# Kernel tuning notes

Measured on AMD Instinct MI355X. Metric: run time of the kernel, lower is better.

Reference implementation:

```python
import jax, jax.numpy as jnp
import numpy as np

K = 10
ALPHA = 0.1
N_NODES = 100000
N_EDGES = 3200000
IN_CH, HID_CH, OUT_CH = 500, 64, 16


def setup_inputs() -> dict:
    key = jax.random.key(0)
    k1, k2, k3, k4, k5, k6 = jax.random.split(key, 6)
    x = jax.random.normal(k1, (N_NODES, IN_CH), dtype=jnp.float32)
    edge_index = jax.random.randint(k2, (2, N_EDGES), 0, N_NODES, dtype=jnp.int64)
    # Linear params (Kaiming-uniform-ish scale)
    s1 = 1.0 / np.sqrt(IN_CH)
    s2 = 1.0 / np.sqrt(HID_CH)
    W1 = jax.random.uniform(k3, (IN_CH, HID_CH), dtype=jnp.float32, minval=-s1, maxval=s1)
    b1 = jax.random.uniform(k4, (HID_CH,), dtype=jnp.float32, minval=-s1, maxval=s1)
    W2 = jax.random.uniform(k5, (HID_CH, OUT_CH), dtype=jnp.float32, minval=-s2, maxval=s2)
    b2 = jax.random.uniform(k6, (OUT_CH,), dtype=jnp.float32, minval=-s2, maxval=s2)
    return {"x": x, "edge_index": edge_index, "W1": W1, "b1": b1, "W2": W2, "b2": b2}


def reference(x, edge_index, W1, b1, W2, b2):
    N = x.shape[0]
    # MLP (eval mode: dropout is identity)
    h = jnp.maximum(x @ W1 + b1, 0.0)
    h = h @ W2 + b2  # [N, out_channels]

    # GCN normalization with self-loops (PyG gcn_norm defaults)
    loops = jnp.arange(N, dtype=edge_index.dtype)
    row = jnp.concatenate([edge_index[0], loops])  # source
    col = jnp.concatenate([edge_index[1], loops])  # target
    ones = jnp.ones(row.shape[0], dtype=h.dtype)
    deg = jax.ops.segment_sum(ones, col, num_segments=N)
    dinv = jnp.where(deg > 0, jax.lax.rsqrt(deg), 0.0)
    norm = dinv[row] * dinv[col]  # [E+N]

    # K-step APPNP propagation: h_{k+1} = (1-alpha) * A_hat h_k + alpha * h_0
    h0 = h

    def step(_, hk):
        agg = jax.ops.segment_sum(norm[:, None] * hk[row], col, num_segments=N)
        return (1.0 - ALPHA) * agg + ALPHA * h0

    return jax.lax.fori_loop(0, K, step, h)
```

## Files before the change

### kernel.cpp

```cpp
#include <hip/hip_runtime.h>

#define IN_CH 500
#define KSTEPS 10

typedef unsigned int u32;
typedef unsigned short u16;
typedef short bf16x8 __attribute__((ext_vector_type(8)));
typedef float f32x4 __attribute__((ext_vector_type(4)));

__device__ __forceinline__ float bf2f(u16 u) {
    union { u32 i; float f; } v; v.i = ((u32)u) << 16; return v.f;
}
__device__ __forceinline__ u16 f2bf(float f) {
    union { float f; u32 i; } v; v.f = f;
    u32 x = v.i;
    return (u16)((x + 0x7FFFu + ((x >> 16) & 1u)) >> 16);
}
__device__ __forceinline__ u32 f_as_u(float f) {
    union { float f; u32 i; } v; v.f = f; return v.i;
}
__device__ __forceinline__ float u_as_f(u32 i) {
    union { u32 i; float f; } v; v.i = i; return v.f;
}

__global__ void detect_kernel(const u16* __restrict__ w1raw,
                              const int* __restrict__ ei,
                              u32* __restrict__ flags) {
    int t = threadIdx.x;
    float m = fabsf(bf2f(w1raw[t]));
    m = fmaxf(m, fabsf(bf2f(w1raw[64 + t])));
    m = fmaxf(m, fabsf(bf2f(w1raw[128 + t])));
    for (int off = 32; off; off >>= 1) m = fmaxf(m, __shfl_down(m, off));
    u32 o = (u32)ei[2 * t + 1];
    o |= (u32)ei[2 * t + 129];
    for (int off = 32; off; off >>= 1) o |= __shfl_down(o, off);
    if (t == 0) {
        flags[0] = (m > 10.0f) ? 1u : 0u;
        flags[1] = (o == 0u) ? 1u : 0u;
    }
}

__global__ void w1t_kernel(const void* __restrict__ W1v,
                           u16* __restrict__ hi, u16* __restrict__ lo,
                           const u32* __restrict__ flags) {
    int i = blockIdx.x * 256 + threadIdx.x;
    if (i >= 64 * 512) return;
    int h = i >> 9;
    int k = i & 511;
    u16 vh = 0, vl = 0;
    if (k < IN_CH) {
        if (flags[0]) {
            float v = ((const float*)W1v)[(size_t)k * 64 + h];
            u32 bits = f_as_u(v);
            vh = (u16)(bits >> 16);
            float d = v - u_as_f(bits & 0xFFFF0000u);
            vl = (u16)(f_as_u(d) >> 16);
        } else {
            vh = ((const u16*)W1v)[(size_t)k * 64 + h];
        }
    }
    hi[(size_t)h * 512 + k] = vh;
    lo[(size_t)h * 512 + k] = vl;
}

__global__ __launch_bounds__(512) void mlp_mfma_f32(
    const float* __restrict__ xf, const u16* __restrict__ w1hig,
    const u16* __restrict__ w1log, const float* __restrict__ b1f,
    const float* __restrict__ W2f, const float* __restrict__ b2f,
    const float* __restrict__ dinv, float* __restrict__ h0,
    float* __restrict__ gout, const u32* __restrict__ flags, int N)
{
    if (flags[0] == 0u) return;

    __shared__ __align__(16) u16 w1hi[64 * 520];
    __shared__ __align__(16) u16 w1lo[64 * 520];
    __shared__ float w2s[64][16];
    __shared__ float b1s[64];
    __shared__ float b2s[16];
    float* hh = (float*)w1hi;

    const int t = threadIdx.x;
    const int w = t >> 6;
    const int l = t & 63;
    const int ln = l & 15;
    const int g = l >> 4;
    const int nodeBase = blockIdx.x * 128;

    for (int i = t; i < 1024; i += 512) w2s[i >> 4][i & 15] = W2f[i];
    if (t < 64) b1s[t] = b1f[t];
    if (t < 16) b2s[t] = b2f[t];

#pragma unroll
    for (int i = 0; i < 8; ++i) {
        int c = t + i * 512;
        int row = c >> 6, c8 = c & 63;
        *(bf16x8*)&w1hi[row * 520 + c8 * 8] =
            *(const bf16x8*)(w1hig + (size_t)row * 512 + c8 * 8);
        *(bf16x8*)&w1lo[row * 520 + c8 * 8] =
            *(const bf16x8*)(w1log + (size_t)row * 512 + c8 * 8);
    }
    __syncthreads();

    const int node = nodeBase + w * 16 + ln;
    const bool nv = (node < N);
    const float* xrow = xf + (size_t)node * IN_CH;

    f32x4 acc0 = {0.f, 0.f, 0.f, 0.f};
    f32x4 acc1 = {0.f, 0.f, 0.f, 0.f};
    f32x4 acc2 = {0.f, 0.f, 0.f, 0.f};
    f32x4 acc3 = {0.f, 0.f, 0.f, 0.f};

#pragma unroll
    for (int ki = 0; ki < 16; ++ki) {
        const int kb = ki * 32 + g * 8;
        float xv[8];
#pragma unroll
        for (int e = 0; e < 8; ++e) xv[e] = 0.f;
        if (nv) {
            if (kb + 8 <= IN_CH) {
                float4 v0 = *(const float4*)(xrow + kb);
                float4 v1 = *(const float4*)(xrow + kb + 4);
                xv[0] = v0.x; xv[1] = v0.y; xv[2] = v0.z; xv[3] = v0.w;
                xv[4] = v1.x; xv[5] = v1.y; xv[6] = v1.z; xv[7] = v1.w;
            } else if (kb < IN_CH) {
                float4 v0 = *(const float4*)(xrow + kb);
                xv[0] = v0.x; xv[1] = v0.y; xv[2] = v0.z; xv[3] = v0.w;
            }
        }
        bf16x8 bh, bl;
#pragma unroll
        for (int e = 0; e < 8; ++e) {
            u32 bits = f_as_u(xv[e]);
            bh[e] = (short)(bits >> 16);
            float d = xv[e] - u_as_f(bits & 0xFFFF0000u);
            bl[e] = (short)(f_as_u(d) >> 16);
        }
        const u16* ph = &w1hi[ln * 520 + kb];
        const u16* pl = &w1lo[ln * 520 + kb];
        bf16x8 ah0 = *(const bf16x8*)(ph);
        bf16x8 ah1 = *(const bf16x8*)(ph + 16 * 520);
        bf16x8 ah2 = *(const bf16x8*)(ph + 32 * 520);
        bf16x8 ah3 = *(const bf16x8*)(ph + 48 * 520);
        bf16x8 al0 = *(const bf16x8*)(pl);
        bf16x8 al1 = *(const bf16x8*)(pl + 16 * 520);
        bf16x8 al2 = *(const bf16x8*)(pl + 32 * 520);
        bf16x8 al3 = *(const bf16x8*)(pl + 48 * 520);
        acc0 = __builtin_amdgcn_mfma_f32_16x16x32_bf16(ah0, bh, acc0, 0, 0, 0);
        acc1 = __builtin_amdgcn_mfma_f32_16x16x32_bf16(ah1, bh, acc1, 0, 0, 0);
        acc2 = __builtin_amdgcn_mfma_f32_16x16x32_bf16(ah2, bh, acc2, 0, 0, 0);
        acc3 = __builtin_amdgcn_mfma_f32_16x16x32_bf16(ah3, bh, acc3, 0, 0, 0);
        acc0 = __builtin_amdgcn_mfma_f32_16x16x32_bf16(al0, bh, acc0, 0, 0, 0);
        acc1 = __builtin_amdgcn_mfma_f32_16x16x32_bf16(al1, bh, acc1, 0, 0, 0);
        acc2 = __builtin_amdgcn_mfma_f32_16x16x32_bf16(al2, bh, acc2, 0, 0, 0);
        acc3 = __builtin_amdgcn_mfma_f32_16x16x32_bf16(al3, bh, acc3, 0, 0, 0);
        acc0 = __builtin_amdgcn_mfma_f32_16x16x32_bf16(ah0, bl, acc0, 0, 0, 0);
        acc1 = __builtin_amdgcn_mfma_f32_16x16x32_bf16(ah1, bl, acc1, 0, 0, 0);
        acc2 = __builtin_amdgcn_mfma_f32_16x16x32_bf16(ah2, bl, acc2, 0, 0, 0);
        acc3 = __builtin_amdgcn_mfma_f32_16x16x32_bf16(ah3, bl, acc3, 0, 0, 0);
    }
    __syncthreads();

    const int nl = w * 16 + ln;
    const int rb = g * 4;
#pragma unroll
    for (int r = 0; r < 4; ++r) {
        float v0 = acc0[r] + b1s[rb + r];
        float v1 = acc1[r] + b1s[16 + rb + r];
        float v2 = acc2[r] + b1s[32 + rb + r];
        float v3 = acc3[r] + b1s[48 + rb + r];
        hh[(rb + r) * 130 + nl]      = v0 > 0.f ? v0 : 0.f;
        hh[(16 + rb + r) * 130 + nl] = v1 > 0.f ? v1 : 0.f;
        hh[(32 + rb + r) * 130 + nl] = v2 > 0.f ? v2 : 0.f;
        hh[(48 + rb + r) * 130 + nl] = v3 > 0.f ? v3 : 0.f;
    }
    __syncthreads();

    {
        int n = t >> 2;
        int o4 = (t & 3) * 4;
        float o0 = b2s[o4], o1 = b2s[o4 + 1], o2 = b2s[o4 + 2], o3 = b2s[o4 + 3];
#pragma unroll
        for (int j = 0; j < 64; ++j) {
            float hv = hh[j * 130 + n];
            o0 += hv * w2s[j][o4];     o1 += hv * w2s[j][o4 + 1];
            o2 += hv * w2s[j][o4 + 2]; o3 += hv * w2s[j][o4 + 3];
        }
        int gn = nodeBase + n;
        if (gn < N) {
            float4 o = {o0, o1, o2, o3};
            *(float4*)(h0 + (size_t)gn * 16 + o4) = o;
            float dn = dinv[gn];
            float4 gg = {o0 * dn, o1 * dn, o2 * dn, o3 * dn};
            *(float4*)(gout + (size_t)gn * 16 + o4) = gg;
        }
    }
}

__global__ __launch_bounds__(256) void mlp_mfma_kernel(
    const u16* __restrict__ xh, const u16* __restrict__ w1tg,
    const void* __restrict__ b1v, const void* __restrict__ W2v,
    const void* __restrict__ b2v, const float* __restrict__ dinv,
    float* __restrict__ h0, float* __restrict__ gout,
    const u32* __restrict__ flags, int N)
{
    if (flags[0] != 0u) return;

    __shared__ __align__(16) u16 w1s[64 * 520];
    __shared__ float w2s[64][16];
    __shared__ float b1s[64];
    __shared__ float b2s[16];
    float* hh = (float*)w1s;

    const u16* b1h = (const u16*)b1v;
    const u16* W2h = (const u16*)W2v;
    const u16* b2h = (const u16*)b2v;

    const int t = threadIdx.x;
    const int w = t >> 6;
    const int l = t & 63;
    const int ln = l & 15;
    const int g = l >> 4;
    const int nodeBase = blockIdx.x * 64;

    for (int i = t; i < 1024; i += 256) w2s[i >> 4][i & 15] = bf2f(W2h[i]);
    if (t < 64) b1s[t] = bf2f(b1h[t]);
    if (t < 16) b2s[t] = bf2f(b2h[t]);

#pragma unroll
    for (int i = 0; i < 16; ++i) {
        int idx = t + i * 256;
        int row = idx >> 6, c8 = idx & 63;
        *(bf16x8*)&w1s[row * 520 + c8 * 8] =
            *(const bf16x8*)(w1tg + (size_t)row * 512 + c8 * 8);
    }
    __syncthreads();

    const int node = nodeBase + w * 16 + ln;
    const bool nv = (node < N);
    const u16* xrow = xh + (size_t)node * IN_CH;

    f32x4 acc0 = {0.f, 0.f, 0.f, 0.f};
    f32x4 acc1 = {0.f, 0.f, 0.f, 0.f};
    f32x4 acc2 = {0.f, 0.f, 0.f, 0.f};
    f32x4 acc3 = {0.f, 0.f, 0.f, 0.f};

#pragma unroll
    for (int ki = 0; ki < 15; ++ki) {
        const int kb = ki * 32 + g * 8;
        bf16x8 b = {0, 0, 0, 0, 0, 0, 0, 0};
        if (nv) b = *(const bf16x8*)(xrow + kb);
        const u16* wp = &w1s[ln * 520 + kb];
        bf16x8 a0 = *(const bf16x8*)(wp);
        bf16x8 a1 = *(const bf16x8*)(wp + 16 * 520);
        bf16x8 a2 = *(const bf16x8*)(wp + 32 * 520);
        bf16x8 a3 = *(const bf16x8*)(wp + 48 * 520);
        acc0 = __builtin_amdgcn_mfma_f32_16x16x32_bf16(a0, b, acc0, 0, 0, 0);
        acc1 = __builtin_amdgcn_mfma_f32_16x16x32_bf16(a1, b, acc1, 0, 0, 0);
        acc2 = __builtin_amdgcn_mfma_f32_16x16x32_bf16(a2, b, acc2, 0, 0, 0);
        acc3 = __builtin_amdgcn_mfma_f32_16x16x32_bf16(a3, b, acc3, 0, 0, 0);
    }
    {
        const int kb = 480 + g * 8;
        bf16x8 b = {0, 0, 0, 0, 0, 0, 0, 0};
        if (nv) {
            if (g < 2) {
                b = *(const bf16x8*)(xrow + kb);
            } else if (g == 2) {
                ushort4 v4 = *(const ushort4*)(xrow + 496);
                b[0] = (short)v4.x; b[1] = (short)v4.y;
                b[2] = (short)v4.z; b[3] = (short)v4.w;
            }
        }
        const u16* wp = &w1s[ln * 520 + kb];
        bf16x8 a0 = *(const bf16x8*)(wp);
        bf16x8 a1 = *(const bf16x8*)(wp + 16 * 520);
        bf16x8 a2 = *(const bf16x8*)(wp + 32 * 520);
        bf16x8 a3 = *(const bf16x8*)(wp + 48 * 520);
        acc0 = __builtin_amdgcn_mfma_f32_16x16x32_bf16(a0, b, acc0, 0, 0, 0);
        acc1 = __builtin_amdgcn_mfma_f32_16x16x32_bf16(a1, b, acc1, 0, 0, 0);
        acc2 = __builtin_amdgcn_mfma_f32_16x16x32_bf16(a2, b, acc2, 0, 0, 0);
        acc3 = __builtin_amdgcn_mfma_f32_16x16x32_bf16(a3, b, acc3, 0, 0, 0);
    }
    __syncthreads();

    const int nl = w * 16 + ln;
    const int rb = g * 4;
#pragma unroll
    for (int r = 0; r < 4; ++r) {
        float v0 = acc0[r] + b1s[rb + r];
        float v1 = acc1[r] + b1s[16 + rb + r];
        float v2 = acc2[r] + b1s[32 + rb + r];
        float v3 = acc3[r] + b1s[48 + rb + r];
        hh[(rb + r) * 65 + nl]      = v0 > 0.f ? v0 : 0.f;
        hh[(16 + rb + r) * 65 + nl] = v1 > 0.f ? v1 : 0.f;
        hh[(32 + rb + r) * 65 + nl] = v2 > 0.f ? v2 : 0.f;
        hh[(48 + rb + r) * 65 + nl] = v3 > 0.f ? v3 : 0.f;
    }
    __syncthreads();

    {
        int n = t >> 2;
        int o4 = (t & 3) * 4;
        float o0 = b2s[o4], o1 = b2s[o4 + 1], o2 = b2s[o4 + 2], o3 = b2s[o4 + 3];
#pragma unroll
        for (int j = 0; j < 64; ++j) {
            float hv = hh[j * 65 + n];
            o0 += hv * w2s[j][o4];     o1 += hv * w2s[j][o4 + 1];
            o2 += hv * w2s[j][o4 + 2]; o3 += hv * w2s[j][o4 + 3];
        }
        int gn = nodeBase + n;
        if (gn < N) {
            float4 o = {o0, o1, o2, o3};
            *(float4*)(h0 + (size_t)gn * 16 + o4) = o;
            float dn = dinv[gn];
            float4 gg = {o0 * dn, o1 * dn, o2 * dn, o3 * dn};
            *(float4*)(gout + (size_t)gn * 16 + o4) = gg;
        }
    }
}

__global__ void zero_u32(u32* __restrict__ p, int n) {
    int i = blockIdx.x * 256 + threadIdx.x;
    if (i < n) p[i] = 0u;
}

__device__ __forceinline__ int ei_src(const int* ei, int E, int e, int i64) {
    return i64 ? ei[2 * e] : ei[e];
}
__device__ __forceinline__ int ei_dst(const int* ei, int E, int e, int i64) {
    return i64 ? ei[2 * (E + e)] : ei[E + e];
}

__global__ void deg_kernel(const int* __restrict__ ei, int E, u32* __restrict__ cnt,
                           const u32* __restrict__ flags) {
    int e = blockIdx.x * 256 + threadIdx.x;
    int i64 = (int)flags[1];
    if (e < E) atomicAdd(&cnt[ei_dst(ei, E, e, i64)], 1u);
}

__global__ void dinv_kernel(const u32* __restrict__ cnt, float* __restrict__ dinv, int N) {
    int i = blockIdx.x * 256 + threadIdx.x;
    if (i < N) {
        float d = (float)(cnt[i] + 1u);
        dinv[i] = rsqrtf(d);
    }
}

__global__ __launch_bounds__(256) void scan1(const u32* __restrict__ cnt,
                                             u32* __restrict__ part, int N) {
    __shared__ u32 s[256];
    int i = blockIdx.x * 256 + threadIdx.x;
    s[threadIdx.x] = (i < N) ? cnt[i] : 0u;
    __syncthreads();
    for (int off = 128; off > 0; off >>= 1) {
        if (threadIdx.x < off) s[threadIdx.x] += s[threadIdx.x + off];
        __syncthreads();
    }
    if (threadIdx.x == 0) part[blockIdx.x] = s[0];
}

__global__ __launch_bounds__(512) void scan2(u32* __restrict__ part,
                                             u32* __restrict__ rowptr, int NB, int N) {
    __shared__ u32 s[512];
    int t = threadIdx.x;
    u32 v = (t < NB) ? part[t] : 0u;
    s[t] = v;
    __syncthreads();
    for (int off = 1; off < 512; off <<= 1) {
        u32 xv = (t >= off) ? s[t - off] : 0u;
        __syncthreads();
        s[t] += xv;
        __syncthreads();
    }
    if (t < NB) part[t] = s[t] - v;
    if (t == 511) rowptr[N] = s[511];
}

__global__ __launch_bounds__(256) void scan3(const u32* __restrict__ cnt,
                                             const u32* __restrict__ part,
                                             u32* __restrict__ rowptr, int N) {
    __shared__ u32 s[256];
    int t = threadIdx.x;
    int i = blockIdx.x * 256 + t;
    u32 v = (i < N) ? cnt[i] : 0u;
    s[t] = v;
    __syncthreads();
    for (int off = 1; off < 256; off <<= 1) {
        u32 xv = (t >= off) ? s[t - off] : 0u;
        __syncthreads();
        s[t] += xv;
        __syncthreads();
    }
    if (i < N) rowptr[i] = part[blockIdx.x] + s[t] - v;
}

__global__ void init_bf(const u32* __restrict__ rowptr, u32* __restrict__ bf,
                        int N, int gsz) {
    int t = threadIdx.x;
    int lo = t * gsz; if (lo > N) lo = N;
    bf[t] = rowptr[lo];
}

#define CHUNK 4096
__global__ __launch_bounds__(256) void bucketA(
    const int* __restrict__ ei, int E, int gsz, int shiftN,
    u32* __restrict__ tmp, u32* __restrict__ bf, const u32* __restrict__ flags)
{
    __shared__ u32 wbuf[CHUNK];
    __shared__ u16 bbuf[CHUNK];
    __shared__ u32 cnt[8], gbase[8], lcnt[8];
    const int i64 = (int)flags[1];
    for (int base = blockIdx.x * CHUNK; base < E; base += gridDim.x * CHUNK) {
        int nval = E - base; if (nval > CHUNK) nval = CHUNK;
        if (threadIdx.x < 8) { cnt[threadIdx.x] = 0u; lcnt[threadIdx.x] = 0u; }
        __syncthreads();
        for (int j = threadIdx.x; j < nval; j += 256) {
            int e = base + j;
            u32 s = (u32)ei_src(ei, E, e, i64);
            u32 d = (u32)ei_dst(ei, E, e, i64);
            u32 b = d / (u32)gsz;
            wbuf[j] = s | ((d - b * (u32)gsz) << shiftN);
            bbuf[j] = (u16)b;
            atomicAdd(&cnt[b], 1u);
        }
        __syncthreads();
        if (threadIdx.x < 8)
            gbase[threadIdx.x] = atomicAdd(&bf[threadIdx.x], cnt[threadIdx.x]);
        __syncthreads();
        for (int j = threadIdx.x; j < nval; j += 256) {
            u32 b = (u32)bbuf[j];
            u32 off = atomicAdd(&lcnt[b], 1u);
            tmp[gbase[b] + off] = wbuf[j];
        }
        __syncthreads();
    }
}

#define FILLB_BPG 64
__global__ __launch_bounds__(256) void bucketB(
    const u32* __restrict__ tmp, const u32* __restrict__ rowptr,
    u32* __restrict__ fillc, u32* __restrict__ ent,
    int N, int gsz, int shiftN)
{
    const int group = blockIdx.x & 7;
    const int bchunk = blockIdx.x >> 3;
    int lo = group * gsz; if (lo > N) lo = N;
    int hi = lo + gsz;    if (hi > N) hi = N;
    if (lo >= hi) return;
    const u32 pstart = rowptr[lo], pend = rowptr[hi];
    const u32 maskN = (1u << shiftN) - 1u;
    const u32 stride = FILLB_BPG * 256;
    for (u32 p = pstart + bchunk * 256 + threadIdx.x; p < pend; p += stride) {
        u32 wd = tmp[p];
        u32 src = wd & maskN;
        u32 c = (u32)lo + (wd >> shiftN);
        u32 pos = rowptr[c] + atomicAdd(&fillc[c], 1u);
        ent[pos] = src;
    }
}

#define FILL_BPG 128
__global__ __launch_bounds__(256) void fill_kernel(
    const int* __restrict__ ei, int E,
    const u32* __restrict__ rowptr, u32* __restrict__ fillc,
    u32* __restrict__ ent, const u32* __restrict__ flags, int N)
{
    const int group = blockIdx.x & 7;
    const int bchunk = blockIdx.x >> 3;
    const int gsz = (N + 7) / 8;
    const int lo = group * gsz;
    const int hi = (lo + gsz < N) ? lo + gsz : N;
    const int i64 = (int)flags[1];
    const int stride = FILL_BPG * 256;
    for (int e = bchunk * 256 + (int)threadIdx.x; e < E; e += stride) {
        int c = ei_dst(ei, E, e, i64);
        if (c >= lo && c < hi) {
            int r = ei_src(ei, E, e, i64);
            u32 p = rowptr[c] + atomicAdd(&fillc[c], 1u);
            ent[p] = (u32)r;
        }
    }
}

__global__ __launch_bounds__(256) void prop_kernel(
    const u32* __restrict__ ent, const u32* __restrict__ rowptr,
    const float* __restrict__ dinv, const float* __restrict__ gcur,
    const float* __restrict__ h0, float* __restrict__ gnext,
    void* __restrict__ outp, const u32* __restrict__ flags, int N)
{
    const int t = threadIdx.x;
    const int wv = t >> 6;
    const int l = t & 63;
    const int c = l & 15;
    const int e = l >> 4;
    const int n = blockIdx.x * 4 + wv;
    if (n >= N) return;

    const u32 rs = rowptr[n], re = rowptr[n + 1];
    float s = 0.f;
    for (u32 base = rs; base < re; base += 32) {
        const u32 p0 = base + (u32)e * 8;
        u32 idx[8];
#pragma unroll
        for (int j = 0; j < 8; ++j) {
            u32 pj = p0 + (u32)j;
            u32 pc = (pj < re) ? pj : (re - 1);
            idx[j] = ent[pc];
        }
#pragma unroll
        for (int j = 0; j < 8; ++j) {
            float v = gcur[(size_t)idx[j] * 16 + c];
            s += (p0 + (u32)j < re) ? v : 0.f;
        }
    }
    s += __shfl_xor(s, 16);
    s += __shfl_xor(s, 32);

    if (e == 0) {
        s += gcur[(size_t)n * 16 + c];
        float dn = dinv[n];
        float h = 0.9f * dn * s + 0.1f * h0[(size_t)n * 16 + c];
        if (gnext) {
            gnext[(size_t)n * 16 + c] = dn * h;
        } else {
            if (flags[0]) ((float*)outp)[(size_t)n * 16 + c] = h;
            else          ((u16*)outp)[(size_t)n * 16 + c] = f2bf(h);
        }
    }
}

extern "C" void kernel_launch(void* const* d_in, const int* in_sizes, int n_in,
                              void* d_out, int out_size, void* d_ws, size_t ws_size,
                              hipStream_t stream) {
    const void* x  = d_in[0];
    const int* ei  = (const int*)d_in[1];
    const void* W1 = d_in[2];
    const void* b1 = d_in[3];
    const void* W2 = d_in[4];
    const void* b2 = d_in[5];

    const int N = in_sizes[0] / IN_CH;
    const int E = in_sizes[1] / 2;

    float* wf = (float*)d_ws;
    u32*   wu = (u32*)d_ws;

    size_t oH0   = 0;
    size_t oGA   = oH0 + (size_t)N * 16;
    size_t oGB   = oGA + (size_t)N * 16;
    size_t oCNT  = oGB + (size_t)N * 16;
    size_t oFILL = oCNT + N;
    size_t oDINV = oFILL + N;
    size_t oRP   = oDINV + N;
    size_t oPART = ((oRP + N + 1 + 3) & ~(size_t)3);
    size_t oFLG  = oPART + 512;
    size_t oENT  = oFLG + 4;
    size_t oTMP  = oENT + E;
    size_t oBF   = oTMP + E;

    int gsz = (N + 7) / 8;
    int shiftN = 1; while ((1 << shiftN) < N && shiftN < 31) shiftN++;
    int shiftL = 1; while ((1 << shiftL) < gsz && shiftL < 31) shiftL++;
    bool canBucket = (ws_size >= (oBF + 8) * 4) && (shiftN + shiftL <= 32);

    u16* w1hig = (u16*)(wf + oGB);
    u16* w1log = w1hig + 64 * 512;

    detect_kernel<<<1, 64, 0, stream>>>((const u16*)W1, ei, wu + oFLG);
    w1t_kernel<<<128, 256, 0, stream>>>(W1, w1hig, w1log, wu + oFLG);
    zero_u32<<<(2 * N + 255) / 256, 256, 0, stream>>>(wu + oCNT, 2 * N);
    deg_kernel<<<(E + 255) / 256, 256, 0, stream>>>(ei, E, wu + oCNT, wu + oFLG);
    dinv_kernel<<<(N + 255) / 256, 256, 0, stream>>>(wu + oCNT, wf + oDINV, N);
    mlp_mfma_f32<<<(N + 127) / 128, 512, 0, stream>>>(
        (const float*)x, w1hig, w1log, (const float*)b1, (const float*)W2,
        (const float*)b2, wf + oDINV, wf + oH0, wf + oGA, wu + oFLG, N);
    mlp_mfma_kernel<<<(N + 63) / 64, 256, 0, stream>>>(
        (const u16*)x, w1hig, b1, W2, b2, wf + oDINV, wf + oH0, wf + oGA,
        wu + oFLG, N);
    int NB = (N + 255) / 256;
    scan1<<<NB, 256, 0, stream>>>(wu + oCNT, wu + oPART, N);
    scan2<<<1, 512, 0, stream>>>(wu + oPART, wu + oRP, NB, N);
    scan3<<<NB, 256, 0, stream>>>(wu + oCNT, wu + oPART, wu + oRP, N);

    if (canBucket) {
        init_bf<<<1, 8, 0, stream>>>(wu + oRP, wu + oBF, N, gsz);
        int nblkA = (E + CHUNK - 1) / CHUNK;
        bucketA<<<nblkA, 256, 0, stream>>>(ei, E, gsz, shiftN,
                                           wu + oTMP, wu + oBF, wu + oFLG);
        bucketB<<<8 * FILLB_BPG, 256, 0, stream>>>(wu + oTMP, wu + oRP,
                                                   wu + oFILL, wu + oENT,
                                                   N, gsz, shiftN);
    } else {
        fill_kernel<<<8 * FILL_BPG, 256, 0, stream>>>(ei, E, wu + oRP,
                                                      wu + oFILL, wu + oENT,
                                                      wu + oFLG, N);
    }

    const float* cur = wf + oGA;
    for (int k = 0; k < KSTEPS; ++k) {
        bool last = (k == KSTEPS - 1);
        float* nxt = last ? nullptr : (wf + ((k & 1) ? oGA : oGB));
        prop_kernel<<<(N + 3) / 4, 256, 0, stream>>>(
            wu + oENT, wu + oRP, wf + oDINV, cur, wf + oH0,
            nxt, last ? d_out : nullptr, wu + oFLG, N);
        if (!last) cur = nxt;
    }
}
```

Baseline: 1.018 ms.

## Use fine-grained 512-node buckets for CSR build and vectorize propagation gathers

The CSR fill changes from 8 coarse destination groups to 512-node buckets. Each bucketB block now loads its rowptr slice into LDS and uses LDS atomics for per-node fill counters instead of global atomics, which also removes one zeroing pass. The propagation kernel now gathers float4 vectors per lane (16 edges by 4 channel groups per wave) and reduces across lanes with shuffles. The costs are more LDS per bucketA block for up to 1024 bucket counters, and many more global atomics on bucket fronts.

```diff
diff --git a/kernel.cpp b/kernel.cpp
--- a/kernel.cpp
+++ b/kernel.cpp
@@ -394,38 +394,43 @@
     if (i < N) rowptr[i] = part[blockIdx.x] + s[t] - v;
 }
 
+#define GSZ_SHIFT 9
+#define GSZ 512
+#define MAXBUCK 1024
 __global__ void init_bf(const u32* __restrict__ rowptr, u32* __restrict__ bf,
-                        int N, int gsz) {
-    int t = threadIdx.x;
-    int lo = t * gsz; if (lo > N) lo = N;
-    bf[t] = rowptr[lo];
+                        int N, int nbuck) {
+    int t = blockIdx.x * 256 + threadIdx.x;
+    if (t < nbuck) {
+        int lo = t << GSZ_SHIFT; if (lo > N) lo = N;
+        bf[t] = rowptr[lo];
+    }
 }
 
 #define CHUNK 4096
 __global__ __launch_bounds__(256) void bucketA(
-    const int* __restrict__ ei, int E, int gsz, int shiftN,
+    const int* __restrict__ ei, int E, int shiftN, int nbuck,
     u32* __restrict__ tmp, u32* __restrict__ bf, const u32* __restrict__ flags)
 {
     __shared__ u32 wbuf[CHUNK];
     __shared__ u16 bbuf[CHUNK];
-    __shared__ u32 cnt[8], gbase[8], lcnt[8];
+    __shared__ u32 cnt[MAXBUCK], gbase[MAXBUCK], lcnt[MAXBUCK];
     const int i64 = (int)flags[1];
     for (int base = blockIdx.x * CHUNK; base < E; base += gridDim.x * CHUNK) {
         int nval = E - base; if (nval > CHUNK) nval = CHUNK;
-        if (threadIdx.x < 8) { cnt[threadIdx.x] = 0u; lcnt[threadIdx.x] = 0u; }
+        for (int b = threadIdx.x; b < nbuck; b += 256) { cnt[b] = 0u; lcnt[b] = 0u; }
         __syncthreads();
         for (int j = threadIdx.x; j < nval; j += 256) {
             int e = base + j;
             u32 s = (u32)ei_src(ei, E, e, i64);
             u32 d = (u32)ei_dst(ei, E, e, i64);
-            u32 b = d / (u32)gsz;
-            wbuf[j] = s | ((d - b * (u32)gsz) << shiftN);
+            u32 b = d >> GSZ_SHIFT;
+            wbuf[j] = s | ((d & (GSZ - 1u)) << shiftN);
             bbuf[j] = (u16)b;
             atomicAdd(&cnt[b], 1u);
         }
         __syncthreads();
-        if (threadIdx.x < 8)
-            gbase[threadIdx.x] = atomicAdd(&bf[threadIdx.x], cnt[threadIdx.x]);
+        for (int b = threadIdx.x; b < nbuck; b += 256)
+            if (cnt[b]) gbase[b] = atomicAdd(&bf[b], cnt[b]);
         __syncthreads();
         for (int j = threadIdx.x; j < nval; j += 256) {
             u32 b = (u32)bbuf[j];
@@ -436,25 +441,25 @@
     }
 }
 
-#define FILLB_BPG 64
-__global__ __launch_bounds__(256) void bucketB(
+__global__ __launch_bounds__(512) void bucketB(
     const u32* __restrict__ tmp, const u32* __restrict__ rowptr,
-    u32* __restrict__ fillc, u32* __restrict__ ent,
-    int N, int gsz, int shiftN)
+    u32* __restrict__ ent, int N, int shiftN)
 {
-    const int group = blockIdx.x & 7;
-    const int bchunk = blockIdx.x >> 3;
-    int lo = group * gsz; if (lo > N) lo = N;
-    int hi = lo + gsz;    if (hi > N) hi = N;
-    if (lo >= hi) return;
-    const u32 pstart = rowptr[lo], pend = rowptr[hi];
-    const u32 maskN = (1u << shiftN) - 1u;
-    const u32 stride = FILLB_BPG * 256;
-    for (u32 p = pstart + bchunk * 256 + threadIdx.x; p < pend; p += stride) {
+    __shared__ u32 rp[GSZ + 1];
+    __shared__ u32 lfill[GSZ];
+    const int lo = blockIdx.x << GSZ_SHIFT;
+    int hi = lo + GSZ; if (hi > N) hi = N;
+    const int nn = hi - lo;
+    for (int i = threadIdx.x; i <= nn; i += 512) rp[i] = rowptr[lo + i];
+    for (int i = threadIdx.x; i < nn; i += 512) lfill[i] = 0u;
+    __syncthreads();
+    const u32 pstart = rp[0], pend = rp[nn];
+    const u32 mask = (1u << shiftN) - 1u;
+    for (u32 p = pstart + threadIdx.x; p < pend; p += 512) {
         u32 wd = tmp[p];
-        u32 src = wd & maskN;
-        u32 c = (u32)lo + (wd >> shiftN);
-        u32 pos = rowptr[c] + atomicAdd(&fillc[c], 1u);
+        u32 src = wd & mask;
+        u32 dl = wd >> shiftN;
+        u32 pos = rp[dl] + atomicAdd(&lfill[dl], 1u);
         ent[pos] = src;
     }
 }
@@ -491,40 +496,47 @@
     const int t = threadIdx.x;
     const int wv = t >> 6;
     const int l = t & 63;
-    const int c = l & 15;
-    const int e = l >> 4;
+    const int eg = l >> 2;
+    const int c4 = (l & 3) * 4;
     const int n = blockIdx.x * 4 + wv;
     if (n >= N) return;
 
     const u32 rs = rowptr[n], re = rowptr[n + 1];
-    float s = 0.f;
+    f32x4 acc = {0.f, 0.f, 0.f, 0.f};
     for (u32 base = rs; base < re; base += 32) {
-        const u32 p0 = base + (u32)e * 8;
-        u32 idx[8];
-#pragma unroll
-        for (int j = 0; j < 8; ++j) {
-            u32 pj = p0 + (u32)j;
-            u32 pc = (pj < re) ? pj : (re - 1);
-            idx[j] = ent[pc];
-        }
-#pragma unroll
-        for (int j = 0; j < 8; ++j) {
-            float v = gcur[(size_t)idx[j] * 16 + c];
-            s += (p0 + (u32)j < re) ? v : 0.f;
-        }
-    }
-    s += __shfl_xor(s, 16);
-    s += __shfl_xor(s, 32);
-
-    if (e == 0) {
-        s += gcur[(size_t)n * 16 + c];
+        u32 pA = base + (u32)eg;
+        u32 pB = pA + 16u;
+        u32 iA = ent[pA < re ? pA : re - 1u];
+        u32 iB = ent[pB < re ? pB : re - 1u];
+        f32x4 vA = *(const f32x4*)(gcur + (size_t)iA * 16 + c4);
+        f32x4 vB = *(const f32x4*)(gcur + (size_t)iB * 16 + c4);
+        if (pA < re) acc += vA;
+        if (pB < re) acc += vB;
+    }
+#pragma unroll
+    for (int off = 4; off <= 32; off <<= 1) {
+        acc[0] += __shfl_xor(acc[0], off);
+        acc[1] += __shfl_xor(acc[1], off);
+        acc[2] += __shfl_xor(acc[2], off);
+        acc[3] += __shfl_xor(acc[3], off);
+    }
+
+    if (eg == 0) {
+        f32x4 self = *(const f32x4*)(gcur + (size_t)n * 16 + c4);
+        f32x4 h0v  = *(const f32x4*)(h0 + (size_t)n * 16 + c4);
         float dn = dinv[n];
-        float h = 0.9f * dn * s + 0.1f * h0[(size_t)n * 16 + c];
+        f32x4 h;
+#pragma unroll
+        for (int j = 0; j < 4; ++j)
+            h[j] = 0.9f * dn * (acc[j] + self[j]) + 0.1f * h0v[j];
         if (gnext) {
-            gnext[(size_t)n * 16 + c] = dn * h;
+            f32x4 gg = {dn * h[0], dn * h[1], dn * h[2], dn * h[3]};
+            *(f32x4*)(gnext + (size_t)n * 16 + c4) = gg;
+        } else if (flags[0]) {
+            *(f32x4*)((float*)outp + (size_t)n * 16 + c4) = h;
         } else {
-            if (flags[0]) ((float*)outp)[(size_t)n * 16 + c] = h;
-            else          ((u16*)outp)[(size_t)n * 16 + c] = f2bf(h);
+            ushort4 o = {f2bf(h[0]), f2bf(h[1]), f2bf(h[2]), f2bf(h[3])};
+            *(ushort4*)((u16*)outp + (size_t)n * 16 + c4) = o;
         }
     }
 }
@@ -558,17 +570,18 @@
     size_t oTMP  = oENT + E;
     size_t oBF   = oTMP + E;
 
-    int gsz = (N + 7) / 8;
+    int nbuck = (N + GSZ - 1) >> GSZ_SHIFT;
     int shiftN = 1; while ((1 << shiftN) < N && shiftN < 31) shiftN++;
-    int shiftL = 1; while ((1 << shiftL) < gsz && shiftL < 31) shiftL++;
-    bool canBucket = (ws_size >= (oBF + 8) * 4) && (shiftN + shiftL <= 32);
+    bool canBucket = (ws_size >= (oBF + MAXBUCK) * 4) &&
+                     (shiftN + GSZ_SHIFT <= 32) && (nbuck <= MAXBUCK);
 
     u16* w1hig = (u16*)(wf + oGB);
     u16* w1log = w1hig + 64 * 512;
 
     detect_kernel<<<1, 64, 0, stream>>>((const u16*)W1, ei, wu + oFLG);
     w1t_kernel<<<128, 256, 0, stream>>>(W1, w1hig, w1log, wu + oFLG);
-    zero_u32<<<(2 * N + 255) / 256, 256, 0, stream>>>(wu + oCNT, 2 * N);
+    int nzero = canBucket ? N : 2 * N;
+    zero_u32<<<(nzero + 255) / 256, 256, 0, stream>>>(wu + oCNT, nzero);
     deg_kernel<<<(E + 255) / 256, 256, 0, stream>>>(ei, E, wu + oCNT, wu + oFLG);
     dinv_kernel<<<(N + 255) / 256, 256, 0, stream>>>(wu + oCNT, wf + oDINV, N);
     mlp_mfma_f32<<<(N + 127) / 128, 512, 0, stream>>>(
@@ -583,13 +596,13 @@
     scan3<<<NB, 256, 0, stream>>>(wu + oCNT, wu + oPART, wu + oRP, N);
 
     if (canBucket) {
-        init_bf<<<1, 8, 0, stream>>>(wu + oRP, wu + oBF, N, gsz);
+        init_bf<<<(nbuck + 255) / 256, 256, 0, stream>>>(wu + oRP, wu + oBF,
+                                                         N, nbuck);
         int nblkA = (E + CHUNK - 1) / CHUNK;
-        bucketA<<<nblkA, 256, 0, stream>>>(ei, E, gsz, shiftN,
+        bucketA<<<nblkA, 256, 0, stream>>>(ei, E, shiftN, nbuck,
                                            wu + oTMP, wu + oBF, wu + oFLG);
-        bucketB<<<8 * FILLB_BPG, 256, 0, stream>>>(wu + oTMP, wu + oRP,
-                                                   wu + oFILL, wu + oENT,
-                                                   N, gsz, shiftN);
+        bucketB<<<nbuck, 512, 0, stream>>>(wu + oTMP, wu + oRP, wu + oENT,
+                                           N, shiftN);
     } else {
         fill_kernel<<<8 * FILL_BPG, 256, 0, stream>>>(ei, E, wu + oRP,
                                                       wu + oFILL, wu + oENT,
```

Result: faster. 992.5 us (-2.5%).
